# Optimization experiments

Hardware: AMD Instinct MI355X
Metric: run time of the kernel (lower is better)

## Reference

```python
import math
import jax, jax.numpy as jnp
import numpy as np

B, S, HID = 2, 2048, 1024
NH, HD = 16, 64            # num heads, head dim (HID = NH*HD)
NB, MAXD = 32, 128         # relative attention buckets / max distance
Q_SCALING = 1.0


def setup_inputs() -> dict:
    key = jax.random.key(0)
    ks = jax.random.split(key, 6)
    return {
        "hidden_states": jax.random.normal(ks[0], (B, S, HID), dtype=jnp.float32),
        "w_qkv": jax.random.normal(ks[1], (HID, 3 * HID), dtype=jnp.float32) * 0.02,
        "b_qkv": jax.random.normal(ks[2], (3 * HID,), dtype=jnp.float32) * 0.02,
        "w_dense": jax.random.normal(ks[3], (HID, HID), dtype=jnp.float32) * 0.02,
        "b_dense": jax.random.normal(ks[4], (HID,), dtype=jnp.float32) * 0.02,
        "rel_attn_table": jax.random.normal(ks[5], (NH, NB), dtype=jnp.float32) * 0.02,
    }


def _relative_position_bucket(q_len, k_len, num_buckets, max_distance):
    # Bidirectional T5-style buckets, matching compute_relative_bias.
    ctx = jnp.arange(q_len, dtype=jnp.int32)[:, None]
    mem = jnp.arange(k_len, dtype=jnp.int32)[None, :]
    rel = mem - ctx                                     # [Q, K]
    nb = num_buckets // 2
    buckets = jnp.where(rel > 0, nb, 0)
    rel = jnp.abs(rel)
    max_exact = nb // 2
    is_small = rel < max_exact
    # log path (clamp to >=1 to avoid log(0); masked by is_small anyway)
    tmp = jnp.log(jnp.maximum(rel, 1).astype(jnp.float32) / max_exact)
    large = tmp / math.log(max_distance / max_exact) * (nb - max_exact)
    large = max_exact + large.astype(jnp.int32)
    large = jnp.minimum(large, nb - 1)
    return buckets + jnp.where(is_small, rel, large)    # [Q, K]


def reference(hidden_states, w_qkv, b_qkv, w_dense, b_dense, rel_attn_table):
    b, s, _ = hidden_states.shape
    qkv = hidden_states @ w_qkv + b_qkv                 # [B, S, 3*HID]
    q, k, v = jnp.split(qkv, 3, axis=-1)
    q = q.reshape(b, s, NH, HD)
    k = k.reshape(b, s, NH, HD)
    v = v.reshape(b, s, NH, HD)

    norm = Q_SCALING * math.sqrt(HD)
    scores = jnp.einsum("bqhd,bkhd->bhqk", q, k) / norm  # [B, H, S, S]

    buckets = _relative_position_bucket(s, s, NB, MAXD)  # [Q, K] int32
    bias = rel_attn_table[:, buckets]                    # [H, Q, K]
    scores = scores + bias[None]

    probs = jax.nn.softmax(scores, axis=-1)
    ctx = jnp.einsum("bhqk,bkhd->bqhd", probs, v).reshape(b, s, HID)
    return ctx @ w_dense + b_dense
```

## Files before the change

### kernel.cpp

```cpp
#include <hip/hip_runtime.h>
#include <hip/hip_bf16.h>
#include <math.h>

#define S_ 2048

typedef __attribute__((ext_vector_type(8))) short bf16x8;
typedef __attribute__((ext_vector_type(4))) float f32x4;
typedef __attribute__((ext_vector_type(8))) unsigned short u16x8;
typedef __attribute__((ext_vector_type(4))) unsigned short u16x4;

__device__ inline unsigned short f2bf(float f) {
  union { float f; unsigned u; } x; x.f = f;
  unsigned r = x.u + 0x7fff + ((x.u >> 16) & 1);
  return (unsigned short)(r >> 16);
}

__device__ __forceinline__ float exp2_raw(float x) {
  float r;
  asm("v_exp_f32 %0, %1" : "=v"(r) : "v"(x));
  return r;
}

__device__ __forceinline__ void gll16(const unsigned short* g, unsigned short* l) {
  __builtin_amdgcn_global_load_lds(
      (const __attribute__((address_space(1))) unsigned int*)g,
      (__attribute__((address_space(3))) unsigned int*)l, 16, 0, 0);
}

__device__ __forceinline__ void transpose_tile(
    const float* __restrict__ in, unsigned short* __restrict__ out,
    int K, int N, int bx, int by, int tid, unsigned short (*tile)[72]) {
  const int k0 = by * 64, n0 = bx * 64;
  const int rr = tid >> 4, cc = (tid & 15) * 4;
#pragma unroll
  for (int p = 0; p < 4; ++p) {
    int k = rr + p * 16;
    float4 v = *(const float4*)&in[(size_t)(k0 + k) * N + n0 + cc];
    tile[k][cc + 0] = f2bf(v.x);
    tile[k][cc + 1] = f2bf(v.y);
    tile[k][cc + 2] = f2bf(v.z);
    tile[k][cc + 3] = f2bf(v.w);
  }
  __syncthreads();
#pragma unroll
  for (int p = 0; p < 4; ++p) {
    int n = rr + p * 16;
    u16x4 o;
    o[0] = tile[cc + 0][n];
    o[1] = tile[cc + 1][n];
    o[2] = tile[cc + 2][n];
    o[3] = tile[cc + 3][n];
    *(u16x4*)&out[(size_t)(n0 + n) * K + k0 + cc] = o;
  }
}

__global__ __launch_bounds__(256) void prologue_kernel(
    const float* __restrict__ hs, unsigned short* __restrict__ hsb,
    const float* __restrict__ w_qkv, unsigned short* __restrict__ wqT,
    const float* __restrict__ w_dense, unsigned short* __restrict__ wdT,
    const float* __restrict__ table, float* __restrict__ biasTab) {
  __shared__ unsigned short tile[64][72];
  const int blk = blockIdx.x;
  const int tid = threadIdx.x;
  if (blk < 2048) {
    int i = blk * 256 + tid;
    float4 a = ((const float4*)hs)[i * 2];
    float4 b = ((const float4*)hs)[i * 2 + 1];
    u16x8 o;
    o[0] = f2bf(a.x); o[1] = f2bf(a.y); o[2] = f2bf(a.z); o[3] = f2bf(a.w);
    o[4] = f2bf(b.x); o[5] = f2bf(b.y); o[6] = f2bf(b.z); o[7] = f2bf(b.w);
    *(u16x8*)&hsb[(size_t)i * 8] = o;
  } else if (blk < 2816) {
    int t = blk - 2048;
    transpose_tile(w_qkv, wqT, 1024, 3072, t % 48, t / 48, tid, tile);
  } else if (blk < 3072) {
    int t = blk - 2816;
    transpose_tile(w_dense, wdT, 1024, 1024, t % 16, t / 16, tid, tile);
  } else {
    int idx = (blk - 3072) * 256 + tid;
    int h = idx >> 12;
    int r = idx & 4095;
    int rel = r - 2047;
    int bucket = rel > 0 ? 16 : 0;
    int ar = rel < 0 ? -rel : rel;
    if (ar < 8) {
      bucket += ar;
    } else {
      float tmp = logf((float)ar / 8.0f);
      float lf = tmp / 2.7725887222397811f * 8.0f;
      int large = 8 + (int)lf;
      bucket += (large < 15 ? large : 15);
    }
    biasTab[idx] = table[h * 32 + bucket] * 1.44269504088896f;
  }
}

template <bool BF16OUT>
__global__ __launch_bounds__(256) void gemm_mfma_kernel(
    const unsigned short* __restrict__ A, const unsigned short* __restrict__ Bt,
    const float* __restrict__ bias, void* __restrict__ Cout,
    unsigned short* __restrict__ vP, int M, int N, int K) {
  __shared__ __align__(16) unsigned short As[128 * 64];
  __shared__ __align__(16) unsigned short Bs[128 * 64];
  const int tid = threadIdx.x;
  const int wave = tid >> 6, lane = tid & 63;
  const int lg = lane >> 4, lr = lane & 15;
  const int nbx = gridDim.x;
  const int flat = blockIdx.y * nbx + blockIdx.x;
  const int cpx = (nbx * gridDim.y) >> 3;
  const int swzid = (flat & 7) * cpx + (flat >> 3);
  const int m0 = (swzid / nbx) * 128, n0 = (swzid % nbx) * 128;
  const int wm = (wave & 1) * 64, wn = (wave >> 1) * 64;

  f32x4 acc[4][4] = {};

  const int rbase = tid >> 3;
  const int lsw = ((tid & 7) ^ (rbase & 7)) * 8;
  const unsigned short* aP[4];
  const unsigned short* bP[4];
  unsigned short* ldsA[4];
  unsigned short* ldsB[4];
#pragma unroll
  for (int g = 0; g < 4; ++g) {
    aP[g] = A + (size_t)(m0 + g * 32 + rbase) * K + lsw;
    bP[g] = Bt + (size_t)(n0 + g * 32 + rbase) * K + lsw;
    ldsA[g] = &As[g * 2048 + (tid & ~63) * 8];
    ldsB[g] = &Bs[g * 2048 + (tid & ~63) * 8];
  }

  for (int kt = 0; kt < K; kt += 64) {
    __syncthreads();
#pragma unroll
    for (int g = 0; g < 4; ++g) {
      gll16(aP[g] + kt, ldsA[g]);
      gll16(bP[g] + kt, ldsB[g]);
    }
    __syncthreads();
#pragma unroll
    for (int kh = 0; kh < 2; ++kh) {
      bf16x8 af[4], bfr[4];
#pragma unroll
      for (int t = 0; t < 4; ++t) {
        const int slot = ((kh * 4 + lg) ^ (lr & 7)) * 8;
        af[t]  = *(const bf16x8*)&As[(wm + t * 16 + lr) * 64 + slot];
        bfr[t] = *(const bf16x8*)&Bs[(wn + t * 16 + lr) * 64 + slot];
      }
#pragma unroll
      for (int i = 0; i < 4; ++i)
#pragma unroll
        for (int j = 0; j < 4; ++j)
          acc[i][j] = __builtin_amdgcn_mfma_f32_16x16x32_bf16(
              af[i], bfr[j], acc[i][j], 0, 0, 0);
    }
  }

  float bv[4];
#pragma unroll
  for (int j = 0; j < 4; ++j) bv[j] = bias[n0 + wn + j * 16 + lr];

  if constexpr (BF16OUT) {
    __syncthreads();
    if (n0 < 2048) {
      unsigned short* rp = &As[wave * 1024];
#pragma unroll
      for (int i = 0; i < 4; ++i) {
#pragma unroll
        for (int j = 0; j < 4; ++j) {
          const int cw = ((j + lg) & 3) * 16 + lr;
#pragma unroll
          for (int r = 0; r < 4; ++r)
            rp[(lg * 4 + r) * 64 + cw] = f2bf(acc[i][j][r] + bv[j]);
        }
#pragma unroll
        for (int pass = 0; pass < 2; ++pass) {
          const int row = pass * 8 + (lane >> 3);
          const int cread = ((((lane & 7) >> 1) + (row >> 2)) & 3) * 16 +
                            (lane & 1) * 8;
          u16x8 v = *(const u16x8*)&rp[row * 64 + cread];
          *(u16x8*)&((unsigned short*)Cout)[
              (size_t)(m0 + wm + i * 16 + row) * N + n0 + wn + (lane & 7) * 8] = v;
        }
      }
    } else {
      unsigned short* R = (wave < 2) ? &As[(wave & 1) * 4096]
                                     : &Bs[(wave & 1) * 4096];
#pragma unroll
      for (int i = 0; i < 4; ++i) {
        const int lsv = (i >> 1) * 4 + lg;
        const int ebase = (i & 1) * 4;
#pragma unroll
        for (int j = 0; j < 4; ++j) {
          const int d = j * 16 + lr;
          const int ps = lsv ^ (d & 7);
          u16x4 o;
#pragma unroll
          for (int r = 0; r < 4; ++r) o[r] = f2bf(acc[i][j][r] + bv[j]);
          *(u16x4*)&R[d * 64 + ps * 8 + ebase] = o;
        }
      }
      const int krow0 = m0 + wm;
      const int bbv = krow0 >> 11;
      const int sbase = krow0 & 2047;
      const int h = ((n0 - 2048) >> 6) + (wave >> 1);
#pragma unroll
      for (int it = 0; it < 8; ++it) {
        const int d = it * 8 + (lane >> 3);
        const int c = lane & 7;
        u16x8 v = *(const u16x8*)&R[d * 64 + c * 8];
        *(u16x8*)&vP[((size_t)((bbv * 16 + h) * 64 + d)) * 2048 +
                     sbase + c * 8] = v;
      }
    }
  } else {
#pragma unroll
    for (int i = 0; i < 4; ++i)
#pragma unroll
      for (int j = 0; j < 4; ++j)
#pragma unroll
        for (int r = 0; r < 4; ++r) {
          int row = m0 + wm + i * 16 + lg * 4 + r;
          int col = n0 + wn + j * 16 + lr;
          ((float*)Cout)[(size_t)row * N + col] = acc[i][j][r] + bv[j];
        }
  }
}

template <bool BF16OUT>
__global__ __launch_bounds__(256) void gemm_mfma64_kernel(
    const unsigned short* __restrict__ A, const unsigned short* __restrict__ Bt,
    const float* __restrict__ bias, void* __restrict__ Cout,
    int M, int N, int K) {
  __shared__ __align__(16) unsigned short As[64 * 64];
  __shared__ __align__(16) unsigned short Bs[128 * 64];
  const int tid = threadIdx.x;
  const int wave = tid >> 6, lane = tid & 63;
  const int lg = lane >> 4, lr = lane & 15;
  const int nbx = gridDim.x;
  const int flat = blockIdx.y * nbx + blockIdx.x;
  const int cpx = (nbx * gridDim.y) >> 3;
  const int swzid = (flat & 7) * cpx + (flat >> 3);
  const int m0 = (swzid / nbx) * 64, n0 = (swzid % nbx) * 128;
  const int wm = (wave & 1) * 32, wn = (wave >> 1) * 64;

  f32x4 acc[2][4] = {};

  const int rbase = tid >> 3;
  const int lsw = ((tid & 7) ^ (rbase & 7)) * 8;
  const unsigned short* aP[2];
  const unsigned short* bP[4];
  unsigned short* ldsA[2];
  unsigned short* ldsB[4];
#pragma unroll
  for (int g = 0; g < 2; ++g) {
    aP[g] = A + (size_t)(m0 + g * 32 + rbase) * K + lsw;
    ldsA[g] = &As[g * 2048 + (tid & ~63) * 8];
  }
#pragma unroll
  for (int g = 0; g < 4; ++g) {
    bP[g] = Bt + (size_t)(n0 + g * 32 + rbase) * K + lsw;
    ldsB[g] = &Bs[g * 2048 + (tid & ~63) * 8];
  }

  for (int kt = 0; kt < K; kt += 64) {
    __syncthreads();
#pragma unroll
    for (int g = 0; g < 2; ++g) gll16(aP[g] + kt, ldsA[g]);
#pragma unroll
    for (int g = 0; g < 4; ++g) gll16(bP[g] + kt, ldsB[g]);
    __syncthreads();
#pragma unroll
    for (int kh = 0; kh < 2; ++kh) {
      bf16x8 af[2], bfr[4];
      const int slotb = ((kh * 4 + lg) ^ (lr & 7)) * 8;
#pragma unroll
      for (int t = 0; t < 2; ++t)
        af[t] = *(const bf16x8*)&As[(wm + t * 16 + lr) * 64 + slotb];
#pragma unroll
      for (int t = 0; t < 4; ++t)
        bfr[t] = *(const bf16x8*)&Bs[(wn + t * 16 + lr) * 64 + slotb];
#pragma unroll
      for (int i = 0; i < 2; ++i)
#pragma unroll
        for (int j = 0; j < 4; ++j)
          acc[i][j] = __builtin_amdgcn_mfma_f32_16x16x32_bf16(
              af[i], bfr[j], acc[i][j], 0, 0, 0);
    }
  }

  float bv[4];
#pragma unroll
  for (int j = 0; j < 4; ++j) bv[j] = bias[n0 + wn + j * 16 + lr];
#pragma unroll
  for (int i = 0; i < 2; ++i) {
#pragma unroll
    for (int j = 0; j < 4; ++j) {
#pragma unroll
      for (int r = 0; r < 4; ++r) {
        int row = m0 + wm + i * 16 + lg * 4 + r;
        int col = n0 + wn + j * 16 + lr;
        float val = acc[i][j][r] + bv[j];
        if constexpr (BF16OUT)
          ((unsigned short*)Cout)[(size_t)row * N + col] = f2bf(val);
        else
          ((float*)Cout)[(size_t)row * N + col] = val;
      }
    }
  }
}

__global__ __launch_bounds__(512) void attn_mfma6_kernel(
    const unsigned short* __restrict__ qkvb, const unsigned short* __restrict__ vP,
    const float* __restrict__ biasTab, unsigned short* __restrict__ ctxb) {
  const int wg0 = blockIdx.x;
  const int wg = (wg0 & 7) * 64 + (wg0 >> 3);
  const int qt = wg & 15;
  const int h  = (wg >> 4) & 15;
  const int bb = wg >> 8;

  const int tid = threadIdx.x;
  const int wave = tid >> 6;
  const int lane = tid & 63;
  const int lg = lane >> 4;
  const int lr = lane & 15;

  __shared__ __align__(16) unsigned short Klds[2][4096];
  __shared__ __align__(16) unsigned short Vlds[2][4096];
  __shared__ float biasW[2][192];

  const int q0 = qt * 128;
  const int qw = q0 + wave * 16;
  const float SCL = 0.125f * 1.44269504088896f;
  const float THR = 11.5415603f;

  bf16x8 qf[2];
#pragma unroll
  for (int kh = 0; kh < 2; ++kh)
    qf[kh] = *(const bf16x8*)(qkvb +
        (size_t)(bb * S_ + qw + lr) * 3072 + h * 64 + kh * 32 + lg * 8);

  float mrun = -1e30f;
  float lpart = 0.f;
  f32x4 ov[4] = {};

  const int kk = tid >> 3, kpb = tid & 7;
  const unsigned short* kptr = qkvb + (size_t)(bb * S_ + kk) * 3072 + 1024 +
                               h * 64 + (kpb ^ (kk & 7)) * 8;
  const unsigned short* vptr = vP + ((size_t)((bb * 16 + h) * 64 + (tid >> 3))) * S_ +
                               (tid & 7) * 8;
  const float* btabH = biasTab + h * 4096 + 2047;

  auto nonuni = [&](int tt) {
    int rl = tt * 64 - q0;
    return !((rl - 127 >= 91) || (rl + 63 <= -91));
  };

  gll16(kptr, &Klds[0][(tid & ~63) * 8]);
  gll16(vptr, &Vlds[0][(tid & ~63) * 8]);
  if (nonuni(0) && tid < 192) biasW[0][tid] = btabH[-q0 - 127 + tid];

  for (int t = 0; t < 32; ++t) {
    const int cur = t & 1;
    __syncthreads();

    if (t < 31) {
      const size_t kadv = (size_t)(t + 1) * 64 * 3072;
      gll16(kptr + kadv, &Klds[cur ^ 1][(tid & ~63) * 8]);
      gll16(vptr + (t + 1) * 64, &Vlds[cur ^ 1][(tid & ~63) * 8]);
      if (nonuni(t + 1) && tid < 192)
        biasW[cur ^ 1][tid] = btabH[(t + 1) * 64 - q0 - 127 + tid];
    }

    f32x4 sc[4] = {};
    __builtin_amdgcn_s_setprio(1);
#pragma unroll
    for (int kt = 0; kt < 4; ++kt) {
      const unsigned short* kr = &Klds[cur][(kt * 16 + lr) * 64];
      bf16x8 kf0 = *(const bf16x8*)(kr + ((lg)     ^ (lr & 7)) * 8);
      bf16x8 kf1 = *(const bf16x8*)(kr + ((4 + lg) ^ (lr & 7)) * 8);
      sc[kt] = __builtin_amdgcn_mfma_f32_16x16x32_bf16(kf0, qf[0], sc[kt], 0, 0, 0);
      sc[kt] = __builtin_amdgcn_mfma_f32_16x16x32_bf16(kf1, qf[1], sc[kt], 0, 0, 0);
    }
    __builtin_amdgcn_s_setprio(0);

    bf16x8 vfr[2][4];
#pragma unroll
    for (int kh = 0; kh < 2; ++kh)
#pragma unroll
      for (int db = 0; db < 4; ++db)
        vfr[kh][db] = *(const bf16x8*)&Vlds[cur][
            (db * 16 + lr) * 64 + ((4 * kh + lg) ^ (lr & 7)) * 8];

    float pp[4][4];
    if (nonuni(t)) {
      const int bidx = 127 + lg * 4 - wave * 16 - lr;
#pragma unroll
      for (int kt = 0; kt < 4; ++kt)
#pragma unroll
        for (int r = 0; r < 4; ++r)
          pp[kt][r] = sc[kt][r] * SCL + biasW[cur][bidx + kt * 16 + r];
    } else {
      const float cb = btabH[t * 64 - q0];
#pragma unroll
      for (int kt = 0; kt < 4; ++kt)
#pragma unroll
        for (int r = 0; r < 4; ++r)
          pp[kt][r] = sc[kt][r] * SCL + cb;
    }

    float mx[8];
#pragma unroll
    for (int i = 0; i < 8; ++i)
      mx[i] = fmaxf(pp[i >> 1][(i & 1) * 2], pp[i >> 1][(i & 1) * 2 + 1]);
    float m01 = fmaxf(mx[0], mx[1]), m23 = fmaxf(mx[2], mx[3]);
    float m45 = fmaxf(mx[4], mx[5]), m67 = fmaxf(mx[6], mx[7]);
    float tm = fmaxf(fmaxf(m01, m23), fmaxf(m45, m67));

    if (!__all(tm <= mrun + THR)) {
      tm = fmaxf(tm, __shfl_xor(tm, 16));
      tm = fmaxf(tm, __shfl_xor(tm, 32));
      float mn = fmaxf(mrun, tm);
      float sfv = exp2_raw(mrun - mn);
      mrun = mn;
      lpart *= sfv;
#pragma unroll
      for (int r = 0; r < 4; ++r) {
        float sq = __shfl(sfv, (lane & 48) | (lg * 4 + r));
#pragma unroll
        for (int db = 0; db < 4; ++db) ov[db][r] *= sq;
      }
    }

#pragma unroll
    for (int kt = 0; kt < 4; ++kt)
#pragma unroll
      for (int r = 0; r < 4; ++r)
        pp[kt][r] = exp2_raw(pp[kt][r] - mrun);
    float s8[8];
#pragma unroll
    for (int i = 0; i < 8; ++i)
      s8[i] = pp[i >> 1][(i & 1) * 2] + pp[i >> 1][(i & 1) * 2 + 1];
    float s01 = s8[0] + s8[1], s23 = s8[2] + s8[3];
    float s45 = s8[4] + s8[5], s67 = s8[6] + s8[7];
    lpart += (s01 + s23) + (s45 + s67);

    union { bf16x8 v; unsigned u[4]; } pk[2];
#pragma unroll
    for (int kh = 0; kh < 2; ++kh) {
      asm("v_cvt_pk_bf16_f32 %0, %1, %2"
          : "=v"(pk[kh].u[0]) : "v"(pp[2 * kh][0]), "v"(pp[2 * kh][1]));
      asm("v_cvt_pk_bf16_f32 %0, %1, %2"
          : "=v"(pk[kh].u[1]) : "v"(pp[2 * kh][2]), "v"(pp[2 * kh][3]));
      asm("v_cvt_pk_bf16_f32 %0, %1, %2"
          : "=v"(pk[kh].u[2]) : "v"(pp[2 * kh + 1][0]), "v"(pp[2 * kh + 1][1]));
      asm("v_cvt_pk_bf16_f32 %0, %1, %2"
          : "=v"(pk[kh].u[3]) : "v"(pp[2 * kh + 1][2]), "v"(pp[2 * kh + 1][3]));
    }

    __builtin_amdgcn_s_setprio(1);
#pragma unroll
    for (int kh = 0; kh < 2; ++kh)
#pragma unroll
      for (int db = 0; db < 4; ++db)
        ov[db] = __builtin_amdgcn_mfma_f32_16x16x32_bf16(
            pk[kh].v, vfr[kh][db], ov[db], 0, 0, 0);
    __builtin_amdgcn_s_setprio(0);
  }

  float lsum = lpart;
  lsum += __shfl_xor(lsum, 16);
  lsum += __shfl_xor(lsum, 32);
  float invl = 1.0f / lsum;
#pragma unroll
  for (int r = 0; r < 4; ++r) {
    float iv = __shfl(invl, (lane & 48) | (lg * 4 + r));
    size_t row = (size_t)(bb * S_ + qw + lg * 4 + r);
#pragma unroll
    for (int db = 0; db < 4; ++db)
      ctxb[row * 1024 + h * 64 + db * 16 + lr] = f2bf(ov[db][r] * iv);
  }
}

extern "C" void kernel_launch(void* const* d_in, const int* in_sizes, int n_in,
                              void* d_out, int out_size, void* d_ws, size_t ws_size,
                              hipStream_t stream) {
  const float* hs      = (const float*)d_in[0];
  const float* w_qkv   = (const float*)d_in[1];
  const float* b_qkv   = (const float*)d_in[2];
  const float* w_dense = (const float*)d_in[3];
  const float* b_dense = (const float*)d_in[4];
  const float* rtab    = (const float*)d_in[5];
  float* out = (float*)d_out;

  char* ws = (char*)d_ws;
  unsigned short* qkvb = (unsigned short*)ws;
  unsigned short* ctxb = (unsigned short*)(ws + (((size_t)24) << 20));
  unsigned short* hsb  = (unsigned short*)(ws + (((size_t)32) << 20));
  unsigned short* wqT  = (unsigned short*)(ws + (((size_t)40) << 20));
  unsigned short* wdT  = (unsigned short*)(ws + (((size_t)46) << 20));
  unsigned short* vP   = (unsigned short*)(ws + (((size_t)48) << 20));
  float* biasTab       = (float*)(ws + (((size_t)56) << 20));

  hipLaunchKernelGGL(prologue_kernel, dim3(3328), dim3(256), 0, stream,
                     hs, hsb, w_qkv, wqT, w_dense, wdT, rtab, biasTab);
  hipLaunchKernelGGL((gemm_mfma_kernel<true>), dim3(24, 32), dim3(256), 0, stream,
                     hsb, wqT, b_qkv, (void*)qkvb, vP, 4096, 3072, 1024);
  hipLaunchKernelGGL(attn_mfma6_kernel, dim3(512), dim3(512), 0, stream,
                     qkvb, vP, biasTab, ctxb);
  hipLaunchKernelGGL((gemm_mfma64_kernel<false>), dim3(8, 64), dim3(256), 0, stream,
                     ctxb, wdT, b_dense, (void*)out, 4096, 1024, 1024);
}
```

Baseline: 127.3 us.

## Double-buffer LDS tiles in both MFMA GEMM kernels with one barrier per step

Both GEMM kernels switch from a single 64-wide K tile loaded and consumed between two barriers to two 32-wide K tiles in LDS, used as ping-pong buffers. The next tile's global-to-LDS loads are issued before the MFMAs on the current tile, so load latency can overlap compute and each iteration needs only one barrier. The XOR swizzle is rebuilt for 32-element rows. The trade-off is twice as many loop iterations, each with less MFMA work to hide load latency behind. The barrier's implicit wait on outstanding loads may also limit how much overlap is actually achieved.

```diff
diff --git a/kernel.cpp b/kernel.cpp
--- a/kernel.cpp
+++ b/kernel.cpp
@@ -100,8 +100,8 @@
     const unsigned short* __restrict__ A, const unsigned short* __restrict__ Bt,
     const float* __restrict__ bias, void* __restrict__ Cout,
     unsigned short* __restrict__ vP, int M, int N, int K) {
-  __shared__ __align__(16) unsigned short As[128 * 64];
-  __shared__ __align__(16) unsigned short Bs[128 * 64];
+  __shared__ __align__(16) unsigned short As[2 * 128 * 32];
+  __shared__ __align__(16) unsigned short Bs[2 * 128 * 32];
   const int tid = threadIdx.x;
   const int wave = tid >> 6, lane = tid & 63;
   const int lg = lane >> 4, lr = lane & 15;
@@ -114,44 +114,50 @@
 
   f32x4 acc[4][4] = {};
 
-  const int rbase = tid >> 3;
-  const int lsw = ((tid & 7) ^ (rbase & 7)) * 8;
-  const unsigned short* aP[4];
-  const unsigned short* bP[4];
-  unsigned short* ldsA[4];
-  unsigned short* ldsB[4];
-#pragma unroll
-  for (int g = 0; g < 4; ++g) {
-    aP[g] = A + (size_t)(m0 + g * 32 + rbase) * K + lsw;
-    bP[g] = Bt + (size_t)(n0 + g * 32 + rbase) * K + lsw;
-    ldsA[g] = &As[g * 2048 + (tid & ~63) * 8];
-    ldsB[g] = &Bs[g * 2048 + (tid & ~63) * 8];
-  }
-
-  for (int kt = 0; kt < K; kt += 64) {
+  const int r0 = tid >> 2;
+  const int sw = ((tid & 3) ^ (r0 & 3)) << 3;
+  const unsigned short* aP0 = A + (size_t)(m0 + r0) * K + sw;
+  const unsigned short* aP1 = A + (size_t)(m0 + 64 + r0) * K + sw;
+  const unsigned short* bP0 = Bt + (size_t)(n0 + r0) * K + sw;
+  const unsigned short* bP1 = Bt + (size_t)(n0 + 64 + r0) * K + sw;
+  unsigned short* ldsA0 = &As[(tid & ~63) * 8];
+  unsigned short* ldsA1 = &As[(256 + (tid & ~63)) * 8];
+  unsigned short* ldsB0 = &Bs[(tid & ~63) * 8];
+  unsigned short* ldsB1 = &Bs[(256 + (tid & ~63)) * 8];
+
+  const int swz = (lg ^ (lr & 3)) << 3;
+  const int NT = K >> 5;
+
+  gll16(aP0, ldsA0);
+  gll16(aP1, ldsA1);
+  gll16(bP0, ldsB0);
+  gll16(bP1, ldsB1);
+
+  for (int ti = 0; ti < NT; ++ti) {
+    const int cur = ti & 1;
     __syncthreads();
-#pragma unroll
-    for (int g = 0; g < 4; ++g) {
-      gll16(aP[g] + kt, ldsA[g]);
-      gll16(bP[g] + kt, ldsB[g]);
-    }
-    __syncthreads();
-#pragma unroll
-    for (int kh = 0; kh < 2; ++kh) {
-      bf16x8 af[4], bfr[4];
-#pragma unroll
-      for (int t = 0; t < 4; ++t) {
-        const int slot = ((kh * 4 + lg) ^ (lr & 7)) * 8;
-        af[t]  = *(const bf16x8*)&As[(wm + t * 16 + lr) * 64 + slot];
-        bfr[t] = *(const bf16x8*)&Bs[(wn + t * 16 + lr) * 64 + slot];
-      }
-#pragma unroll
-      for (int i = 0; i < 4; ++i)
-#pragma unroll
-        for (int j = 0; j < 4; ++j)
-          acc[i][j] = __builtin_amdgcn_mfma_f32_16x16x32_bf16(
-              af[i], bfr[j], acc[i][j], 0, 0, 0);
-    }
+    if (ti + 1 < NT) {
+      const int kt = (ti + 1) << 5;
+      const int nb = (cur ^ 1) * 4096;
+      gll16(aP0 + kt, ldsA0 + nb);
+      gll16(aP1 + kt, ldsA1 + nb);
+      gll16(bP0 + kt, ldsB0 + nb);
+      gll16(bP1 + kt, ldsB1 + nb);
+    }
+    const unsigned short* Ab = &As[cur * 4096];
+    const unsigned short* Bb = &Bs[cur * 4096];
+    bf16x8 af[4], bfr[4];
+#pragma unroll
+    for (int t = 0; t < 4; ++t) {
+      af[t]  = *(const bf16x8*)&Ab[(wm + t * 16 + lr) * 32 + swz];
+      bfr[t] = *(const bf16x8*)&Bb[(wn + t * 16 + lr) * 32 + swz];
+    }
+#pragma unroll
+    for (int i = 0; i < 4; ++i)
+#pragma unroll
+      for (int j = 0; j < 4; ++j)
+        acc[i][j] = __builtin_amdgcn_mfma_f32_16x16x32_bf16(
+            af[i], bfr[j], acc[i][j], 0, 0, 0);
   }
 
   float bv[4];
@@ -230,8 +236,8 @@
     const unsigned short* __restrict__ A, const unsigned short* __restrict__ Bt,
     const float* __restrict__ bias, void* __restrict__ Cout,
     int M, int N, int K) {
-  __shared__ __align__(16) unsigned short As[64 * 64];
-  __shared__ __align__(16) unsigned short Bs[128 * 64];
+  __shared__ __align__(16) unsigned short As[2 * 64 * 32];
+  __shared__ __align__(16) unsigned short Bs[2 * 128 * 32];
   const int tid = threadIdx.x;
   const int wave = tid >> 6, lane = tid & 63;
   const int lg = lane >> 4, lr = lane & 15;
@@ -244,47 +250,46 @@
 
   f32x4 acc[2][4] = {};
 
-  const int rbase = tid >> 3;
-  const int lsw = ((tid & 7) ^ (rbase & 7)) * 8;
-  const unsigned short* aP[2];
-  const unsigned short* bP[4];
-  unsigned short* ldsA[2];
-  unsigned short* ldsB[4];
-#pragma unroll
-  for (int g = 0; g < 2; ++g) {
-    aP[g] = A + (size_t)(m0 + g * 32 + rbase) * K + lsw;
-    ldsA[g] = &As[g * 2048 + (tid & ~63) * 8];
-  }
-#pragma unroll
-  for (int g = 0; g < 4; ++g) {
-    bP[g] = Bt + (size_t)(n0 + g * 32 + rbase) * K + lsw;
-    ldsB[g] = &Bs[g * 2048 + (tid & ~63) * 8];
-  }
-
-  for (int kt = 0; kt < K; kt += 64) {
+  const int r0 = tid >> 2;
+  const int sw = ((tid & 3) ^ (r0 & 3)) << 3;
+  const unsigned short* aP  = A + (size_t)(m0 + r0) * K + sw;
+  const unsigned short* bP0 = Bt + (size_t)(n0 + r0) * K + sw;
+  const unsigned short* bP1 = Bt + (size_t)(n0 + 64 + r0) * K + sw;
+  unsigned short* ldsA  = &As[(tid & ~63) * 8];
+  unsigned short* ldsB0 = &Bs[(tid & ~63) * 8];
+  unsigned short* ldsB1 = &Bs[(256 + (tid & ~63)) * 8];
+
+  const int swz = (lg ^ (lr & 3)) << 3;
+  const int NT = K >> 5;
+
+  gll16(aP, ldsA);
+  gll16(bP0, ldsB0);
+  gll16(bP1, ldsB1);
+
+  for (int ti = 0; ti < NT; ++ti) {
+    const int cur = ti & 1;
     __syncthreads();
-#pragma unroll
-    for (int g = 0; g < 2; ++g) gll16(aP[g] + kt, ldsA[g]);
-#pragma unroll
-    for (int g = 0; g < 4; ++g) gll16(bP[g] + kt, ldsB[g]);
-    __syncthreads();
-#pragma unroll
-    for (int kh = 0; kh < 2; ++kh) {
-      bf16x8 af[2], bfr[4];
-      const int slotb = ((kh * 4 + lg) ^ (lr & 7)) * 8;
-#pragma unroll
-      for (int t = 0; t < 2; ++t)
-        af[t] = *(const bf16x8*)&As[(wm + t * 16 + lr) * 64 + slotb];
-#pragma unroll
-      for (int t = 0; t < 4; ++t)
-        bfr[t] = *(const bf16x8*)&Bs[(wn + t * 16 + lr) * 64 + slotb];
-#pragma unroll
-      for (int i = 0; i < 2; ++i)
-#pragma unroll
-        for (int j = 0; j < 4; ++j)
-          acc[i][j] = __builtin_amdgcn_mfma_f32_16x16x32_bf16(
-              af[i], bfr[j], acc[i][j], 0, 0, 0);
-    }
+    if (ti + 1 < NT) {
+      const int kt = (ti + 1) << 5;
+      gll16(aP + kt, ldsA + (cur ^ 1) * 2048);
+      gll16(bP0 + kt, ldsB0 + (cur ^ 1) * 4096);
+      gll16(bP1 + kt, ldsB1 + (cur ^ 1) * 4096);
+    }
+    const unsigned short* Ab = &As[cur * 2048];
+    const unsigned short* Bb = &Bs[cur * 4096];
+    bf16x8 af[2], bfr[4];
+#pragma unroll
+    for (int t = 0; t < 2; ++t)
+      af[t] = *(const bf16x8*)&Ab[(wm + t * 16 + lr) * 32 + swz];
+#pragma unroll
+    for (int t = 0; t < 4; ++t)
+      bfr[t] = *(const bf16x8*)&Bb[(wn + t * 16 + lr) * 32 + swz];
+#pragma unroll
+    for (int i = 0; i < 2; ++i)
+#pragma unroll
+      for (int j = 0; j < 4; ++j)
+        acc[i][j] = __builtin_amdgcn_mfma_f32_16x16x32_bf16(
+            af[i], bfr[j], acc[i][j], 0, 0, 0);
   }
 
   float bv[4];
```

After: 133.2 us. +4.6%, slower.
